# Performance work log

Hardware: AMD Instinct MI355X
Metric: run time of the kernel (lower is better)

Reference implementation:

```python
import jax, jax.numpy as jnp
import numpy as np

B, T, D, E, F, K = 8, 2048, 1024, 8, 4096, 2

def setup_inputs() -> dict:
    key = jax.random.key(0)
    ks = jax.random.split(key, 5)
    s = 1.0 / np.sqrt(D)
    return {
        "tokens": jax.random.normal(ks[0], (B, T, D), jnp.float32),
        "gate_w": jax.random.normal(ks[1], (E, D), jnp.float32) * s,
        "gate_b": jnp.zeros((E,), jnp.float32),
        "w1": jax.random.normal(ks[2], (E, F, D), jnp.float32) * s,
        "b1": jnp.zeros((E, F), jnp.float32),
        "w2": jax.random.normal(ks[3], (E, D, F), jnp.float32) * (1.0 / np.sqrt(F)),
        "b2": jnp.zeros((E, D), jnp.float32),
    }

def reference(tokens, gate_w, gate_b, w1, b1, w2, b2):
    # gate: [B,T,E]
    logits = jnp.einsum('btd,ed->bte', tokens, gate_w) + gate_b
    # top-k over experts: weights/ixs [B,T,K]
    weights, expert_ixs = jax.lax.top_k(logits, K)
    # NOTE: original torch code applies softmax over dim=1 (the token axis),
    # not the top-k axis; reproduce faithfully.
    weights = jax.nn.softmax(weights, axis=1)
    # combined per-expert gate weight [B,T,E] (additive combine is equivalent
    # to the per-slot scatter-add in the torch loop)
    onehot = jax.nn.one_hot(expert_ixs, E, dtype=weights.dtype)  # [B,T,K,E]
    gate_per_expert = jnp.einsum('btk,btke->bte', weights, onehot)
    results = jnp.zeros_like(tokens)
    for e in range(E):  # small fixed expert count
        h = jax.nn.relu(jnp.einsum('btd,fd->btf', tokens, w1[e]) + b1[e])
        y = jnp.einsum('btf,df->btd', h, w2[e]) + b2[e]
        results = results + gate_per_expert[..., e:e + 1] * y
    return results
```

## Files before the change

kernel.cpp:

```cpp
#include <hip/hip_runtime.h>

#define BT 16384
#define DD 1024
#define NE 8
#define FF 4096

typedef unsigned short u16;
using v8s = __attribute__((ext_vector_type(8))) short;
using v4f = __attribute__((ext_vector_type(4))) float;

__device__ inline u16 f2bf(float f){ union{float f; unsigned int u;} v; v.f=f; unsigned r=v.u+0x7fffu+((v.u>>16)&1u); return (u16)(r>>16); }
__device__ inline unsigned pk(float x, float y){
  union{float f; unsigned u;} a, b; a.f=x; b.f=y;
  return __builtin_amdgcn_perm(b.u, a.u, 0x07060302u);
}
__device__ inline uint2 pk4(float4 v){
  uint2 r; r.x = pk(v.x, v.y); r.y = pk(v.z, v.w); return r;
}

__global__ __launch_bounds__(256) void k_gate(const float* __restrict__ tok, const float* __restrict__ gw,
                                              const float* __restrict__ gb, float* __restrict__ lp,
                                              int* __restrict__ eArr, int* __restrict__ ctrl){
  int wid = threadIdx.x >> 6, lane = threadIdx.x & 63;
  int t = blockIdx.x*4 + wid;
  const float* xp = tok + (size_t)t*DD + lane*16;
  float x[16];
  {
    float4 q0=*(const float4*)xp, q1=*(const float4*)(xp+4), q2=*(const float4*)(xp+8), q3=*(const float4*)(xp+12);
    x[0]=q0.x;x[1]=q0.y;x[2]=q0.z;x[3]=q0.w; x[4]=q1.x;x[5]=q1.y;x[6]=q1.z;x[7]=q1.w;
    x[8]=q2.x;x[9]=q2.y;x[10]=q2.z;x[11]=q2.w; x[12]=q3.x;x[13]=q3.y;x[14]=q3.z;x[15]=q3.w;
  }
  float lg[NE];
  #pragma unroll
  for(int e=0;e<NE;e++){
    const float* wp = gw + e*DD + lane*16;
    float4 q0=*(const float4*)wp, q1=*(const float4*)(wp+4), q2=*(const float4*)(wp+8), q3=*(const float4*)(wp+12);
    float w[16]={q0.x,q0.y,q0.z,q0.w,q1.x,q1.y,q1.z,q1.w,q2.x,q2.y,q2.z,q2.w,q3.x,q3.y,q3.z,q3.w};
    float s=0.f;
    #pragma unroll
    for(int i=0;i<16;i++) s += x[i]*w[i];
    #pragma unroll
    for(int off=32;off;off>>=1) s += __shfl_xor(s,off);
    lg[e] = s + gb[e];
  }
  if(lane==0){
    float l0=-3e38f,l1=-3e38f; int e0=0,e1=0;
    #pragma unroll
    for(int e=0;e<NE;e++){ float v=lg[e];
      if(v>l0){l1=l0;e1=e0;l0=v;e0=e;} else if(v>l1){l1=v;e1=e;} }
    lp[t]=l0; lp[BT+t]=l1;
    eArr[t*2]=e0; eArr[t*2+1]=e1;
    atomicAdd(&ctrl[e0],1); atomicAdd(&ctrl[e1],1);
  }
}

__global__ __launch_bounds__(256) void k_smstats(const float* __restrict__ lp, float* __restrict__ mv,
                                                 float* __restrict__ sv){
  __shared__ float sm[256];
  int idx=blockIdx.x; int b=idx>>1, k=idx&1;
  const float* p = lp + k*BT + b*2048;
  int tid=threadIdx.x;
  float m=-3e38f;
  #pragma unroll
  for(int i=0;i<8;i++) m=fmaxf(m, p[tid+i*256]);
  sm[tid]=m; __syncthreads();
  for(int s=128;s;s>>=1){ if(tid<s) sm[tid]=fmaxf(sm[tid],sm[tid+s]); __syncthreads(); }
  float mx=sm[0]; __syncthreads();
  float su=0.f;
  #pragma unroll
  for(int i=0;i<8;i++) su += expf(p[tid+i*256]-mx);
  sm[tid]=su; __syncthreads();
  for(int s=128;s;s>>=1){ if(tid<s) sm[tid]+=sm[tid+s]; __syncthreads(); }
  if(tid==0){ mv[idx]=mx; sv[idx]=sm[0]; }
}

__global__ void k_prefix(int* ctrl){
  if(threadIdx.x==0 && blockIdx.x==0){
    int run=0;
    for(int e=0;e<NE;e++){ ctrl[16+e]=run; ctrl[8+e]=run; run+=ctrl[e]; }
  }
}

__global__ __launch_bounds__(256) void k_assign(const float* __restrict__ lp, const int* __restrict__ eArr,
                                                const float* __restrict__ mv, const float* __restrict__ sv,
                                                int* __restrict__ ctrl, int* __restrict__ token_of,
                                                float* __restrict__ g_row){
  int t = blockIdx.x*256 + threadIdx.x;
  int b = t >> 11;
  #pragma unroll
  for(int k=0;k<2;k++){
    float l = lp[k*BT+t];
    float g = expf(l - mv[b*2+k]) / sv[b*2+k];
    int e = eArr[t*2+k];
    int row = atomicAdd(&ctrl[8+e],1);
    token_of[row]=t; g_row[row]=g;
  }
}

__global__ __launch_bounds__(256,2) void k_ffn1(const float* __restrict__ tok, const float* __restrict__ w1,
                                                const float* __restrict__ b1, u16* __restrict__ H,
                                                const int* __restrict__ ctrl, const int* __restrict__ token_of,
                                                int split_off, int FS){
  __shared__ u16 lsA[128*72];
  __shared__ u16 lsB[128*72];
  int e = blockIdx.z;
  int ne = ctrl[e];
  int m0 = blockIdx.x*128;
  if(m0 >= ne) return;
  int rbase = ctrl[16+e];
  int n0 = blockIdx.y*128;
  int tid=threadIdx.x, lane=tid&63, wid=tid>>6;
  int wm=wid&1, wn=wid>>1;
  int srow = tid>>1, shalf = tid&1;
  int gm = m0 + srow;
  int trow = (gm<ne)? token_of[rbase+gm] : 0;
  const float* aG = tok + (size_t)trow*DD + shalf*32;
  const float* bG = w1 + ((size_t)e*FF + split_off + n0 + srow)*DD + shalf*32;
  v4f acc[4][4];
  #pragma unroll
  for(int i=0;i<4;i++){
    #pragma unroll
    for(int j=0;j<4;j++) acc[i][j]=(v4f)(0.f); }
  for(int k0=0;k0<DD;k0+=64){
    uint2 pa[8], pb[8];
    #pragma unroll
    for(int i=0;i<8;i++) pa[i]=pk4(*(const float4*)(aG+k0+i*4));
    #pragma unroll
    for(int i=0;i<8;i++) pb[i]=pk4(*(const float4*)(bG+k0+i*4));
    __syncthreads();
    int sb = srow*72 + shalf*32;
    #pragma unroll
    for(int i=0;i<4;i++){
      *(uint4*)&lsA[sb+i*8] = make_uint4(pa[2*i].x,pa[2*i].y,pa[2*i+1].x,pa[2*i+1].y);
      *(uint4*)&lsB[sb+i*8] = make_uint4(pb[2*i].x,pb[2*i].y,pb[2*i+1].x,pb[2*i+1].y);
    }
    __syncthreads();
    #pragma unroll
    for(int kk=0; kk<64; kk+=32){
      v8s af[4], bf[4];
      #pragma unroll
      for(int mi=0;mi<4;mi++) af[mi] = *(const v8s*)&lsA[(wm*64+mi*16+(lane&15))*72 + kk + (lane>>4)*8];
      #pragma unroll
      for(int ni=0;ni<4;ni++) bf[ni] = *(const v8s*)&lsB[(wn*64+ni*16+(lane&15))*72 + kk + (lane>>4)*8];
      #pragma unroll
      for(int mi=0;mi<4;mi++)
        #pragma unroll
        for(int ni=0;ni<4;ni++)
          acc[mi][ni] = __builtin_amdgcn_mfma_f32_16x16x32_bf16(af[mi],bf[ni],acc[mi][ni],0,0,0);
    }
  }
  int rq = (lane>>4)*4;
  #pragma unroll
  for(int mi=0;mi<4;mi++){
    int rowb = m0 + wm*64 + mi*16 + rq;
    #pragma unroll
    for(int r=0;r<4;r++){
      int gmr = rowb + r;
      if(gmr >= ne) continue;
      size_t hoff = (size_t)(rbase+gmr)*FS;
      #pragma unroll
      for(int ni=0;ni<4;ni++){
        int col = wn*64+ni*16+(lane&15);
        int fi = n0 + col;
        float v = acc[mi][ni][r] + b1[(size_t)e*FF + split_off + fi];
        v = fmaxf(v,0.f);
        H[hoff + fi] = f2bf(v);
      }
    }
  }
}

__global__ __launch_bounds__(256,2) void k_ffn2(const u16* __restrict__ H, const float* __restrict__ w2,
                                                const float* __restrict__ b2, float* __restrict__ outF,
                                                const int* __restrict__ ctrl, const int* __restrict__ token_of,
                                                const float* __restrict__ g_row, int split_off, int FS, int addb){
  __shared__ u16 lsA[128*72];
  __shared__ u16 lsB[128*72];
  int e = blockIdx.z;
  int ne = ctrl[e];
  int m0 = blockIdx.x*128;
  if(m0 >= ne) return;
  int rbase = ctrl[16+e];
  int n0 = blockIdx.y*128;
  int tid=threadIdx.x, lane=tid&63, wid=tid>>6;
  int wm=wid&1, wn=wid>>1;
  int srow = tid>>1, shalf = tid&1;
  int arow = rbase + m0 + srow; if(arow > 2*BT-1) arow = 2*BT-1;
  const u16* aG = H + (size_t)arow*FS + shalf*32;
  const float* bG = w2 + ((size_t)e*DD + n0 + srow)*FF + split_off + shalf*32;
  v4f acc[4][4];
  #pragma unroll
  for(int i=0;i<4;i++){
    #pragma unroll
    for(int j=0;j<4;j++) acc[i][j]=(v4f)(0.f); }
  for(int k0=0;k0<FS;k0+=64){
    uint4 a0=*(const uint4*)(aG+k0), a1=*(const uint4*)(aG+k0+8),
          a2=*(const uint4*)(aG+k0+16), a3=*(const uint4*)(aG+k0+24);
    uint2 pb[8];
    #pragma unroll
    for(int i=0;i<8;i++) pb[i]=pk4(*(const float4*)(bG+k0+i*4));
    __syncthreads();
    int sb = srow*72 + shalf*32;
    *(uint4*)&lsA[sb+0]=a0; *(uint4*)&lsA[sb+8]=a1; *(uint4*)&lsA[sb+16]=a2; *(uint4*)&lsA[sb+24]=a3;
    #pragma unroll
    for(int i=0;i<4;i++)
      *(uint4*)&lsB[sb+i*8] = make_uint4(pb[2*i].x,pb[2*i].y,pb[2*i+1].x,pb[2*i+1].y);
    __syncthreads();
    #pragma unroll
    for(int kk=0; kk<64; kk+=32){
      v8s af[4], bf[4];
      #pragma unroll
      for(int mi=0;mi<4;mi++) af[mi] = *(const v8s*)&lsA[(wm*64+mi*16+(lane&15))*72 + kk + (lane>>4)*8];
      #pragma unroll
      for(int ni=0;ni<4;ni++) bf[ni] = *(const v8s*)&lsB[(wn*64+ni*16+(lane&15))*72 + kk + (lane>>4)*8];
      #pragma unroll
      for(int mi=0;mi<4;mi++)
        #pragma unroll
        for(int ni=0;ni<4;ni++)
          acc[mi][ni] = __builtin_amdgcn_mfma_f32_16x16x32_bf16(af[mi],bf[ni],acc[mi][ni],0,0,0);
    }
  }
  int rq = (lane>>4)*4;
  #pragma unroll
  for(int mi=0;mi<4;mi++){
    int rowb = m0 + wm*64 + mi*16 + rq;
    #pragma unroll
    for(int r=0;r<4;r++){
      int gmr = rowb + r;
      if(gmr >= ne) continue;
      int grow = rbase + gmr;
      int t = token_of[grow];
      float g = g_row[grow];
      #pragma unroll
      for(int ni=0;ni<4;ni++){
        int col = wn*64+ni*16+(lane&15);
        int d = n0 + col;
        float v = acc[mi][ni][r]*g;
        if(addb) v += g*b2[e*DD + d];
        unsafeAtomicAdd(&outF[(size_t)t*DD + d], v);
      }
    }
  }
}

extern "C" void kernel_launch(void* const* d_in, const int* in_sizes, int n_in,
                              void* d_out, int out_size, void* d_ws, size_t ws_size,
                              hipStream_t stream){
  (void)in_sizes; (void)n_in; (void)out_size;
  const float* tok=(const float*)d_in[0];
  const float* gw =(const float*)d_in[1];
  const float* gb =(const float*)d_in[2];
  const float* w1 =(const float*)d_in[3];
  const float* b1 =(const float*)d_in[4];
  const float* w2 =(const float*)d_in[5];
  const float* b2 =(const float*)d_in[6];
  float* outF=(float*)d_out;

  const size_t TAIL = (size_t)4*1024*1024;
  int S=0; size_t HB=0;
  for(int s=1;s<=32;s<<=1){
    size_t hb=(size_t)2*BT*(FF/s)*2;
    if(hb + TAIL <= ws_size){ S=s; HB=hb; break; }
  }
  if(!S) return;

  char* p=(char*)d_ws;
  u16*  H      = (u16*)p;
  float* lp    = (float*)(p + HB);
  float* g_row = lp + 2*BT;
  int*  token_of = (int*)(g_row + 2*BT);
  int*  eArr     = token_of + 2*BT;
  int*  ctrl     = eArr + 2*BT;
  float* mv      = (float*)(ctrl + 64);
  float* sv      = mv + 16;

  hipMemsetAsync(ctrl, 0, 256, stream);
  hipMemsetAsync(outF, 0, (size_t)BT*DD*4, stream);

  k_gate   <<<dim3(BT/4), dim3(256), 0, stream>>>(tok, gw, gb, lp, eArr, ctrl);
  k_smstats<<<dim3(16),   dim3(256), 0, stream>>>(lp, mv, sv);
  k_prefix <<<dim3(1),    dim3(64),  0, stream>>>(ctrl);
  k_assign <<<dim3(BT/256), dim3(256), 0, stream>>>(lp, eArr, mv, sv, ctrl, token_of, g_row);

  int FS = FF/S;
  for(int s=0;s<S;s++){
    k_ffn1<<<dim3(48, FS/128, NE), dim3(256), 0, stream>>>(tok, w1, b1, H, ctrl, token_of, s*FS, FS);
    k_ffn2<<<dim3(48, DD/128, NE), dim3(256), 0, stream>>>(H, w2, b2, outF, ctrl, token_of, g_row, s*FS, FS, s==0?1:0);
  }
}
```

Baseline: 3.036 ms.

## Pre-convert tokens and weights to bf16 and stage tiles via direct global-to-LDS loads

Adds a conversion pass that turns tokens, w1 and w2 into bf16 copies in the workspace at the start of each call. The FFN GEMMs then read bf16 through global_load_lds, which writes straight into LDS without going through registers. The LDS layout changes to column-chunk-major 8-element groups, so fragment reads index differently. This removes the per-tile fp32 loads and in-register packing and halves the bytes each GEMM tile reads. In exchange it pays an extra full pass over the weights every call and needs more workspace, which may force a larger F-split.

```diff
diff --git a/kernel.cpp b/kernel.cpp
--- a/kernel.cpp
+++ b/kernel.cpp
@@ -10,12 +10,19 @@
 using v4f = __attribute__((ext_vector_type(4))) float;
 
 __device__ inline u16 f2bf(float f){ union{float f; unsigned int u;} v; v.f=f; unsigned r=v.u+0x7fffu+((v.u>>16)&1u); return (u16)(r>>16); }
-__device__ inline unsigned pk(float x, float y){
-  union{float f; unsigned u;} a, b; a.f=x; b.f=y;
-  return __builtin_amdgcn_perm(b.u, a.u, 0x07060302u);
-}
-__device__ inline uint2 pk4(float4 v){
-  uint2 r; r.x = pk(v.x, v.y); r.y = pk(v.z, v.w); return r;
+
+__device__ inline void gload16(const u16* g, u16* l){
+  __builtin_amdgcn_global_load_lds((const __attribute__((address_space(1))) unsigned int*)g,
+                                   (__attribute__((address_space(3))) unsigned int*)l, 16, 0, 0);
+}
+
+__global__ __launch_bounds__(256) void k_cvt(const float* __restrict__ in, u16* __restrict__ out, long n){
+  long i = ((long)blockIdx.x*256 + threadIdx.x)*8;
+  if(i >= n) return;
+  float4 a = *(const float4*)(in+i);
+  float4 b = *(const float4*)(in+i+4);
+  *(ushort4*)(out+i)   = make_ushort4(f2bf(a.x), f2bf(a.y), f2bf(a.z), f2bf(a.w));
+  *(ushort4*)(out+i+4) = make_ushort4(f2bf(b.x), f2bf(b.y), f2bf(b.z), f2bf(b.w));
 }
 
 __global__ __launch_bounds__(256) void k_gate(const float* __restrict__ tok, const float* __restrict__ gw,
@@ -97,51 +104,55 @@
   }
 }
 
-__global__ __launch_bounds__(256,2) void k_ffn1(const float* __restrict__ tok, const float* __restrict__ w1,
-                                                const float* __restrict__ b1, u16* __restrict__ H,
-                                                const int* __restrict__ ctrl, const int* __restrict__ token_of,
-                                                int split_off, int FS){
-  __shared__ u16 lsA[128*72];
-  __shared__ u16 lsB[128*72];
+
+__global__ __launch_bounds__(256) void k_ffn1(const u16* __restrict__ tokb, const u16* __restrict__ w1b,
+                                              const float* __restrict__ b1, u16* __restrict__ H,
+                                              const int* __restrict__ ctrl, const int* __restrict__ token_of,
+                                              int split_off, int FS){
+  __shared__ u16 lsA[8192];
+  __shared__ u16 lsB[8192];
   int e = blockIdx.z;
   int ne = ctrl[e];
   int m0 = blockIdx.x*128;
   if(m0 >= ne) return;
   int rbase = ctrl[16+e];
   int n0 = blockIdx.y*128;
-  int tid=threadIdx.x, lane=tid&63, wid=tid>>6;
-  int wm=wid&1, wn=wid>>1;
-  int srow = tid>>1, shalf = tid&1;
-  int gm = m0 + srow;
-  int trow = (gm<ne)? token_of[rbase+gm] : 0;
-  const float* aG = tok + (size_t)trow*DD + shalf*32;
-  const float* bG = w1 + ((size_t)e*FF + split_off + n0 + srow)*DD + shalf*32;
+  int tid=threadIdx.x, lane=tid&63, wave=tid>>6;
+  int wm=wave&1, wn=wave>>1;
+  const u16* aP[4]; const u16* bP[4]; u16* lA[4]; u16* lB[4];
+  #pragma unroll
+  for(int j=0;j<4;j++){
+    int Wj = wave*256 + j*64;
+    int row = (Wj & 127) + lane;
+    int c16 = Wj >> 7;
+    int gm = m0 + row; if(gm > ne-1) gm = ne-1;
+    int tr = token_of[rbase + gm];
+    aP[j] = tokb + (size_t)tr*DD + c16*8;
+    bP[j] = w1b + ((size_t)e*FF + split_off + n0 + row)*DD + c16*8;
+    lA[j] = lsA + (size_t)Wj*8;
+    lB[j] = lsB + (size_t)Wj*8;
+  }
   v4f acc[4][4];
   #pragma unroll
   for(int i=0;i<4;i++){
     #pragma unroll
     for(int j=0;j<4;j++) acc[i][j]=(v4f)(0.f); }
+  int q = lane>>4, ml = lane&15;
   for(int k0=0;k0<DD;k0+=64){
-    uint2 pa[8], pb[8];
-    #pragma unroll
-    for(int i=0;i<8;i++) pa[i]=pk4(*(const float4*)(aG+k0+i*4));
-    #pragma unroll
-    for(int i=0;i<8;i++) pb[i]=pk4(*(const float4*)(bG+k0+i*4));
     __syncthreads();
-    int sb = srow*72 + shalf*32;
-    #pragma unroll
-    for(int i=0;i<4;i++){
-      *(uint4*)&lsA[sb+i*8] = make_uint4(pa[2*i].x,pa[2*i].y,pa[2*i+1].x,pa[2*i+1].y);
-      *(uint4*)&lsB[sb+i*8] = make_uint4(pb[2*i].x,pb[2*i].y,pb[2*i+1].x,pb[2*i+1].y);
+    #pragma unroll
+    for(int j=0;j<4;j++){
+      gload16(aP[j], lA[j]); gload16(bP[j], lB[j]);
+      aP[j]+=64; bP[j]+=64;
     }
     __syncthreads();
     #pragma unroll
-    for(int kk=0; kk<64; kk+=32){
+    for(int kk=0;kk<2;kk++){
       v8s af[4], bf[4];
       #pragma unroll
-      for(int mi=0;mi<4;mi++) af[mi] = *(const v8s*)&lsA[(wm*64+mi*16+(lane&15))*72 + kk + (lane>>4)*8];
-      #pragma unroll
-      for(int ni=0;ni<4;ni++) bf[ni] = *(const v8s*)&lsB[(wn*64+ni*16+(lane&15))*72 + kk + (lane>>4)*8];
+      for(int mi=0;mi<4;mi++) af[mi] = *(const v8s*)&lsA[(kk*4+q)*1024 + (wm*64+mi*16+ml)*8];
+      #pragma unroll
+      for(int ni=0;ni<4;ni++) bf[ni] = *(const v8s*)&lsB[(kk*4+q)*1024 + (wn*64+ni*16+ml)*8];
       #pragma unroll
       for(int mi=0;mi<4;mi++)
         #pragma unroll
@@ -149,7 +160,7 @@
           acc[mi][ni] = __builtin_amdgcn_mfma_f32_16x16x32_bf16(af[mi],bf[ni],acc[mi][ni],0,0,0);
     }
   }
-  int rq = (lane>>4)*4;
+  int rq = q*4;
   #pragma unroll
   for(int mi=0;mi<4;mi++){
     int rowb = m0 + wm*64 + mi*16 + rq;
@@ -160,7 +171,7 @@
       size_t hoff = (size_t)(rbase+gmr)*FS;
       #pragma unroll
       for(int ni=0;ni<4;ni++){
-        int col = wn*64+ni*16+(lane&15);
+        int col = wn*64+ni*16+ml;
         int fi = n0 + col;
         float v = acc[mi][ni][r] + b1[(size_t)e*FF + split_off + fi];
         v = fmaxf(v,0.f);
@@ -170,49 +181,53 @@
   }
 }
 
-__global__ __launch_bounds__(256,2) void k_ffn2(const u16* __restrict__ H, const float* __restrict__ w2,
-                                                const float* __restrict__ b2, float* __restrict__ outF,
-                                                const int* __restrict__ ctrl, const int* __restrict__ token_of,
-                                                const float* __restrict__ g_row, int split_off, int FS, int addb){
-  __shared__ u16 lsA[128*72];
-  __shared__ u16 lsB[128*72];
+__global__ __launch_bounds__(256) void k_ffn2(const u16* __restrict__ H, const u16* __restrict__ w2b,
+                                              const float* __restrict__ b2, float* __restrict__ outF,
+                                              const int* __restrict__ ctrl, const int* __restrict__ token_of,
+                                              const float* __restrict__ g_row, int split_off, int FS, int addb){
+  __shared__ u16 lsA[8192];
+  __shared__ u16 lsB[8192];
   int e = blockIdx.z;
   int ne = ctrl[e];
   int m0 = blockIdx.x*128;
   if(m0 >= ne) return;
   int rbase = ctrl[16+e];
   int n0 = blockIdx.y*128;
-  int tid=threadIdx.x, lane=tid&63, wid=tid>>6;
-  int wm=wid&1, wn=wid>>1;
-  int srow = tid>>1, shalf = tid&1;
-  int arow = rbase + m0 + srow; if(arow > 2*BT-1) arow = 2*BT-1;
-  const u16* aG = H + (size_t)arow*FS + shalf*32;
-  const float* bG = w2 + ((size_t)e*DD + n0 + srow)*FF + split_off + shalf*32;
+  int tid=threadIdx.x, lane=tid&63, wave=tid>>6;
+  int wm=wave&1, wn=wave>>1;
+  const u16* aP[4]; const u16* bP[4]; u16* lA[4]; u16* lB[4];
+  #pragma unroll
+  for(int j=0;j<4;j++){
+    int Wj = wave*256 + j*64;
+    int row = (Wj & 127) + lane;
+    int c16 = Wj >> 7;
+    int gm = m0 + row; if(gm > ne-1) gm = ne-1;
+    aP[j] = H + (size_t)(rbase+gm)*FS + c16*8;
+    bP[j] = w2b + ((size_t)e*DD + n0 + row)*FF + split_off + c16*8;
+    lA[j] = lsA + (size_t)Wj*8;
+    lB[j] = lsB + (size_t)Wj*8;
+  }
   v4f acc[4][4];
   #pragma unroll
   for(int i=0;i<4;i++){
     #pragma unroll
     for(int j=0;j<4;j++) acc[i][j]=(v4f)(0.f); }
+  int q = lane>>4, ml = lane&15;
   for(int k0=0;k0<FS;k0+=64){
-    uint4 a0=*(const uint4*)(aG+k0), a1=*(const uint4*)(aG+k0+8),
-          a2=*(const uint4*)(aG+k0+16), a3=*(const uint4*)(aG+k0+24);
-    uint2 pb[8];
-    #pragma unroll
-    for(int i=0;i<8;i++) pb[i]=pk4(*(const float4*)(bG+k0+i*4));
     __syncthreads();
-    int sb = srow*72 + shalf*32;
-    *(uint4*)&lsA[sb+0]=a0; *(uint4*)&lsA[sb+8]=a1; *(uint4*)&lsA[sb+16]=a2; *(uint4*)&lsA[sb+24]=a3;
-    #pragma unroll
-    for(int i=0;i<4;i++)
-      *(uint4*)&lsB[sb+i*8] = make_uint4(pb[2*i].x,pb[2*i].y,pb[2*i+1].x,pb[2*i+1].y);
+    #pragma unroll
+    for(int j=0;j<4;j++){
+      gload16(aP[j], lA[j]); gload16(bP[j], lB[j]);
+      aP[j]+=64; bP[j]+=64;
+    }
     __syncthreads();
     #pragma unroll
-    for(int kk=0; kk<64; kk+=32){
+    for(int kk=0;kk<2;kk++){
       v8s af[4], bf[4];
       #pragma unroll
-      for(int mi=0;mi<4;mi++) af[mi] = *(const v8s*)&lsA[(wm*64+mi*16+(lane&15))*72 + kk + (lane>>4)*8];
-      #pragma unroll
-      for(int ni=0;ni<4;ni++) bf[ni] = *(const v8s*)&lsB[(wn*64+ni*16+(lane&15))*72 + kk + (lane>>4)*8];
+      for(int mi=0;mi<4;mi++) af[mi] = *(const v8s*)&lsA[(kk*4+q)*1024 + (wm*64+mi*16+ml)*8];
+      #pragma unroll
+      for(int ni=0;ni<4;ni++) bf[ni] = *(const v8s*)&lsB[(kk*4+q)*1024 + (wn*64+ni*16+ml)*8];
       #pragma unroll
       for(int mi=0;mi<4;mi++)
         #pragma unroll
@@ -220,7 +235,7 @@
           acc[mi][ni] = __builtin_amdgcn_mfma_f32_16x16x32_bf16(af[mi],bf[ni],acc[mi][ni],0,0,0);
     }
   }
-  int rq = (lane>>4)*4;
+  int rq = q*4;
   #pragma unroll
   for(int mi=0;mi<4;mi++){
     int rowb = m0 + wm*64 + mi*16 + rq;
@@ -233,7 +248,7 @@
       float g = g_row[grow];
       #pragma unroll
       for(int ni=0;ni<4;ni++){
-        int col = wn*64+ni*16+(lane&15);
+        int col = wn*64+ni*16+ml;
         int d = n0 + col;
         float v = acc[mi][ni][r]*g;
         if(addb) v += g*b2[e*DD + d];
@@ -256,26 +271,37 @@
   const float* b2 =(const float*)d_in[6];
   float* outF=(float*)d_out;
 
-  const size_t TAIL = (size_t)4*1024*1024;
+  const long NTOK = (long)BT*DD;
+  const long NW   = (long)NE*FF*DD;
+  const size_t CONV = (size_t)(NTOK + 2*NW)*2;
+  const size_t CTL  = 1<<20;
   int S=0; size_t HB=0;
   for(int s=1;s<=32;s<<=1){
     size_t hb=(size_t)2*BT*(FF/s)*2;
-    if(hb + TAIL <= ws_size){ S=s; HB=hb; break; }
+    if(CONV + CTL + hb <= ws_size){ S=s; HB=hb; break; }
   }
   if(!S) return;
 
   char* p=(char*)d_ws;
-  u16*  H      = (u16*)p;
-  float* lp    = (float*)(p + HB);
+  u16* tokb = (u16*)p;
+  u16* w1b  = tokb + NTOK;
+  u16* w2b  = w1b + NW;
+  char* q   = (char*)(w2b + NW);
+  float* lp    = (float*)q;
   float* g_row = lp + 2*BT;
   int*  token_of = (int*)(g_row + 2*BT);
   int*  eArr     = token_of + 2*BT;
   int*  ctrl     = eArr + 2*BT;
   float* mv      = (float*)(ctrl + 64);
   float* sv      = mv + 16;
+  u16*  H        = (u16*)(q + CTL);
 
   hipMemsetAsync(ctrl, 0, 256, stream);
   hipMemsetAsync(outF, 0, (size_t)BT*DD*4, stream);
+
+  k_cvt<<<dim3((unsigned)(NTOK/8/256)), dim3(256), 0, stream>>>(tok, tokb, NTOK);
+  k_cvt<<<dim3((unsigned)(NW/8/256)),   dim3(256), 0, stream>>>(w1, w1b, NW);
+  k_cvt<<<dim3((unsigned)(NW/8/256)),   dim3(256), 0, stream>>>(w2, w2b, NW);
 
   k_gate   <<<dim3(BT/4), dim3(256), 0, stream>>>(tok, gw, gb, lp, eArr, ctrl);
   k_smstats<<<dim3(16),   dim3(256), 0, stream>>>(lp, mv, sv);
@@ -284,7 +310,7 @@
 
   int FS = FF/S;
   for(int s=0;s<S;s++){
-    k_ffn1<<<dim3(48, FS/128, NE), dim3(256), 0, stream>>>(tok, w1, b1, H, ctrl, token_of, s*FS, FS);
-    k_ffn2<<<dim3(48, DD/128, NE), dim3(256), 0, stream>>>(H, w2, b2, outF, ctrl, token_of, g_row, s*FS, FS, s==0?1:0);
-  }
-}
+    k_ffn1<<<dim3(48, FS/128, NE), dim3(256), 0, stream>>>(tokb, w1b, b1, H, ctrl, token_of, s*FS, FS);
+    k_ffn2<<<dim3(48, DD/128, NE), dim3(256), 0, stream>>>(H, w2b, b2, outF, ctrl, token_of, g_row, s*FS, FS, s==0?1:0);
+  }
+}
```

Result: faster. 2.446 ms (-19.4%).
